# Optimization experiments

Hardware: AMD Instinct MI355X
Metric: run time of the kernel (lower is better)

## Reference

```python
import jax, jax.numpy as jnp
import numpy as np
import math

B, Q, CQ = 2, 2048, 512
H, D = 8, 64  # no_heads, c_hidden

def setup_inputs() -> dict:
    key = jax.random.key(0)
    ks = jax.random.split(key, 8)
    s = 0.02
    return {
        "q_x": jax.random.normal(ks[0], (B, Q, CQ), jnp.float32),
        "kv_x": jax.random.normal(ks[1], (B, Q, CQ), jnp.float32),
        "bias": jax.random.normal(ks[2], (B, 1, Q, Q), jnp.float32),
        "w_qkv": jax.random.normal(ks[3], (3 * H * D, CQ), jnp.float32) * s,
        "w_o": jax.random.normal(ks[4], (CQ, H * D), jnp.float32) * s,
        "b_o": jnp.zeros((CQ,), jnp.float32),
        "w_g": jax.random.normal(ks[5], (H * D, CQ), jnp.float32) * s,
        "b_g": jnp.zeros((H * D,), jnp.float32),
    }

def reference(q_x, kv_x, bias, w_qkv, w_o, b_o, w_g, b_g):
    # Fused QKV projection from q_x (kv_x is unused by the original module's _prep_qkv)
    qkv = jnp.einsum('bqc,ec->bqe', q_x, w_qkv)  # [B,Q,3*H*D]
    q, k, v = jnp.split(qkv, 3, axis=-1)
    q = q.reshape(B, Q, H, D) / math.sqrt(D)
    k = k.reshape(B, Q, H, D)
    v = v.reshape(B, Q, H, D)
    # scores + additive pairwise bias, softmax over keys
    scores = jnp.einsum('bqhd,bkhd->bhqk', q, k) + bias  # [B,H,Q,K]
    attn = jax.nn.softmax(scores, axis=-1)
    o = jnp.einsum('bhqk,bkhd->bqhd', attn, v)  # [B,Q,H,D]
    # sigmoid gating
    g = jax.nn.sigmoid(jnp.einsum('bqc,ec->bqe', q_x, w_g) + b_g).reshape(B, Q, H, D)
    o = o * g
    # output projection
    o = o.reshape(B, Q, H * D)
    return jnp.einsum('bqe,ce->bqc', o, w_o) + b_o
```

## Files before the change

### kernel.cpp

```cpp
#include <hip/hip_runtime.h>
#include <math.h>

#define B_  2
#define Q_  2048
#define CQ_ 512
#define H_  8
#define D_  64
#define M_  (B_*Q_)
#define L2E 1.44269504088896f

typedef __bf16 bf16;
typedef __bf16 bf16x4 __attribute__((ext_vector_type(4)));
typedef __bf16 bf16x8 __attribute__((ext_vector_type(8)));
typedef float  f32x4  __attribute__((ext_vector_type(4)));
typedef float  f32x16 __attribute__((ext_vector_type(16)));
typedef unsigned int u32x2 __attribute__((ext_vector_type(2)));

__device__ __forceinline__ void gl_lds16(const bf16* g, bf16* l) {
    __builtin_amdgcn_global_load_lds(
        (const __attribute__((address_space(1))) unsigned int*)g,
        (__attribute__((address_space(3))) unsigned int*)l, 16, 0, 0);
}

__device__ __forceinline__ unsigned int cvtpk_bf16(float lo, float hi) {
    unsigned int r;
    asm("v_cvt_pk_bf16_f32 %0, %1, %2" : "=v"(r) : "v"(lo), "v"(hi));
    return r;
}

#define S0 (4096*512)
#define S1 (1536*512)
#define S2 (512*512)
#define S3 (512*512)
#define NCV ((S0 + S1 + S2 + S3) / (256 * 8))
__global__ __launch_bounds__(256)
void convert_kernel(const float* __restrict__ qx, const float* __restrict__ wqkv,
                    const float* __restrict__ wg, const float* __restrict__ wo,
                    const float* __restrict__ bias,
                    bf16* __restrict__ qxb, bf16* __restrict__ wcat,
                    bf16* __restrict__ wob, float* __restrict__ bT)
{
    __shared__ float lds[2048];
    const int bx = blockIdx.x;
    const int t  = threadIdx.x;
    if (bx < NCV) {
        const long long e = ((long long)bx * 256 + t) * 8;
        const float* src; bf16* dst;
        if (e < S0)                { src = qx + e;                  dst = qxb + e; }
        else if (e < S0 + S1)      { src = wqkv + (e - S0);         dst = wcat + (e - S0); }
        else if (e < S0 + S1 + S2) { src = wg + (e - S0 - S1);      dst = wcat + S1 + (e - S0 - S1); }
        else                       { src = wo + (e - S0 - S1 - S2); dst = wob + (e - S0 - S1 - S2); }
        const float4 a = *(const float4*)(src);
        const float4 b = *(const float4*)(src + 4);
        bf16x8 v;
        v[0] = (bf16)a.x; v[1] = (bf16)a.y; v[2] = (bf16)a.z; v[3] = (bf16)a.w;
        v[4] = (bf16)b.x; v[5] = (bf16)b.y; v[6] = (bf16)b.z; v[7] = (bf16)b.w;
        *(bf16x8*)dst = v;
    } else {
        const int x = bx - NCV;
        const int b = x >> 11, q32 = (x >> 5) & 63, kt = x & 31;
        const int qo = t >> 3, kc = (t & 7) * 8;
        const float* src = bias + ((size_t)b * Q_ + q32 * 32 + qo) * Q_ + kt * 64 + kc;
        const float4 a = *(const float4*)src;
        const float4 c = *(const float4*)(src + 4);
        const float v[8] = {a.x, a.y, a.z, a.w, c.x, c.y, c.z, c.w};
        #pragma unroll
        for (int j2 = 0; j2 < 8; ++j2) {
            const int ko = kc + j2;
            const int i  = (ko >> 5) * 4 + ((ko >> 3) & 3);
            const int b5 = (ko >> 2) & 1;
            const int j  = ko & 3;
            lds[i * 256 + b5 * 128 + qo * 4 + j] = v[j2] * L2E;
        }
        __syncthreads();
        float* outp = bT + ((size_t)(b * 64 + q32) * 32 + kt) * 2048 + t * 8;
        *(float4*)(outp)     = *(const float4*)(lds + t * 8);
        *(float4*)(outp + 4) = *(const float4*)(lds + t * 8 + 4);
    }
}

template<int BM, int BN>
__global__ __launch_bounds__(256)
void gemm_bf16(const bf16* __restrict__ A, const bf16* __restrict__ W,
               const float* __restrict__ bvec,
               bf16* __restrict__ qb, bf16* __restrict__ kb, bf16* __restrict__ vb,
               bf16* __restrict__ gb)
{
    constexpr int MI = BM / 32, NJ = BN / 32;
    __shared__ __align__(16) bf16 As[BM * 32];
    __shared__ __align__(16) bf16 Bs[BN * 32];

    const int t = threadIdx.x;
    const int w = t >> 6, lane = t & 63;
    const int l15 = lane & 15, quad = lane >> 4;
    const int wm = w & 1, wn = w >> 1;
    const int bm = blockIdx.x * BM;
    const int bn = blockIdx.y * BN;
    const bool swapped = ((bn >> 9) != 2);

    f32x4 acc[MI][NJ] = {};

    const int rr = t >> 2;
    const int cc = (t & 3) * 8;

    for (int k0 = 0; k0 < 512; k0 += 32) {
        #pragma unroll
        for (int i = 0; i < BM / 64; ++i)
            gl_lds16(A + (size_t)(bm + i * 64 + rr) * 512 + k0 + cc,
                     As + (i * 64 + w * 16) * 32);
        #pragma unroll
        for (int i = 0; i < BN / 64; ++i)
            gl_lds16(W + (size_t)(bn + i * 64 + rr) * 512 + k0 + cc,
                     Bs + (i * 64 + w * 16) * 32);
        __asm__ volatile("s_waitcnt vmcnt(0)" ::: "memory");
        __syncthreads();

        bf16x8 af[MI], bfr[NJ];
        #pragma unroll
        for (int i = 0; i < MI; ++i)
            af[i] = *(const bf16x8*)(As + (wm * (BM / 2) + i * 16 + l15) * 32 + quad * 8);
        #pragma unroll
        for (int j = 0; j < NJ; ++j)
            bfr[j] = *(const bf16x8*)(Bs + (wn * (BN / 2) + j * 16 + l15) * 32 + quad * 8);
        if (swapped) {
            #pragma unroll
            for (int i = 0; i < MI; ++i)
                #pragma unroll
                for (int j = 0; j < NJ; ++j)
                    acc[i][j] = __builtin_amdgcn_mfma_f32_16x16x32_bf16(bfr[j], af[i], acc[i][j], 0, 0, 0);
        } else {
            #pragma unroll
            for (int i = 0; i < MI; ++i)
                #pragma unroll
                for (int j = 0; j < NJ; ++j)
                    acc[i][j] = __builtin_amdgcn_mfma_f32_16x16x32_bf16(af[i], bfr[j], acc[i][j], 0, 0, 0);
        }
        __syncthreads();
    }

    if (swapped) {
        #pragma unroll
        for (int i = 0; i < MI; ++i) {
            const int m = bm + wm * (BM / 2) + i * 16 + l15;
            const int b = m >> 11, qq = m & 2047;
            #pragma unroll
            for (int j = 0; j < NJ; ++j) {
                const int n0 = bn + wn * (BN / 2) + j * 16 + quad * 4;
                const f32x4 cv = acc[i][j];
                const int part = n0 >> 9;
                if (part == 0) {
                    const int h = (n0 >> 6) & 7, d0 = n0 & 63;
                    bf16x4 q4;
                    #pragma unroll
                    for (int r = 0; r < 4; ++r) q4[r] = (bf16)(cv[r] * (0.125f * L2E));
                    *(bf16x4*)(qb + (size_t)(b * H_ + h) * (Q_ * D_) + (size_t)qq * 64 + d0) = q4;
                } else if (part == 1) {
                    const int h = (n0 >> 6) & 7, d0 = n0 & 63;
                    const size_t off = (size_t)(b * H_ + h) * (Q_ * D_)
                        + (qq >> 6) * 4096 + ((qq >> 5) & 1) * 2048
                        + (d0 >> 4) * 512 + ((d0 >> 3) & 1) * 256
                        + (qq & 31) * 8 + (d0 & 7);
                    bf16x4 k4;
                    #pragma unroll
                    for (int r = 0; r < 4; ++r) k4[r] = (bf16)cv[r];
                    *(bf16x4*)(kb + off) = k4;
                } else {
                    const int gcol = n0 & 511;
                    const float4 bv4 = *(const float4*)(bvec + gcol);
                    bf16x4 g4;
                    g4[0] = (bf16)(1.f / (1.f + __expf(-(cv[0] + bv4.x))));
                    g4[1] = (bf16)(1.f / (1.f + __expf(-(cv[1] + bv4.y))));
                    g4[2] = (bf16)(1.f / (1.f + __expf(-(cv[2] + bv4.z))));
                    g4[3] = (bf16)(1.f / (1.f + __expf(-(cv[3] + bv4.w))));
                    *(bf16x4*)(gb + (size_t)m * 512 + gcol) = g4;
                }
            }
        }
    } else {
        #pragma unroll
        for (int i = 0; i < MI; ++i) {
            const int m0 = bm + wm * (BM / 2) + i * 16 + quad * 4;
            const int b = m0 >> 11, qq0 = m0 & 2047;
            #pragma unroll
            for (int j = 0; j < NJ; ++j) {
                const int n = bn + wn * (BN / 2) + j * 16 + l15;
                const int h = (n >> 6) & 7, d = n & 63;
                const size_t off = (size_t)(b * H_ + h) * (Q_ * D_)
                    + (qq0 >> 6) * 4096 + (d >> 5) * 2048
                    + ((qq0 & 63) >> 4) * 512 + ((qq0 >> 3) & 1) * 256
                    + (d & 31) * 8 + (qq0 & 7);
                bf16x4 v4;
                #pragma unroll
                for (int r = 0; r < 4; ++r) v4[r] = (bf16)acc[i][j][r];
                *(bf16x4*)(vb + off) = v4;
            }
        }
    }
}

__global__ __launch_bounds__(256, 3)
void attn_part(const bf16* __restrict__ qb, const bf16* __restrict__ kf,
               const bf16* __restrict__ vf, const float* __restrict__ bT,
               bf16* __restrict__ po, float2* __restrict__ ml)
{
    __shared__ __align__(16) bf16 Ks[2][4096];
    __shared__ __align__(16) bf16 Vs[2][4096];

    const int tid  = threadIdx.x;
    const int wv   = tid >> 6, lane = tid & 63;
    const int l31  = lane & 31, b5 = lane >> 5;
    const int x    = blockIdx.x;
    const int bh   = ((x & 7) << 1) | (x >> 3);
    const int b    = bh >> 3;
    const int qg   = blockIdx.y * 128 + wv * 32 + l31;
    const int ks   = blockIdx.z;
    const int t0   = ks * 11;
    const int nt   = (ks < 2) ? 11 : 10;

    const bf16* qp = qb + ((size_t)bh * Q_ + qg) * D_;
    bf16x8 bq[4];
    #pragma unroll
    for (int c = 0; c < 4; ++c)
        bq[c] = *(const bf16x8*)(qp + c * 16 + b5 * 8);

    f32x16 acc[2] = {};
    float m_run = -INFINITY, l_run = 0.f;

    const bf16*  kfb  = kf + (size_t)bh * (Q_ * D_) + (size_t)t0 * 4096;
    const bf16*  vfb  = vf + (size_t)bh * (Q_ * D_) + (size_t)t0 * 4096;
    const int q32 = blockIdx.y * 4 + wv;
    const float* brow = bT + (((size_t)b * 64 + q32) * 32 + t0) * 2048;

    f32x4 nb[8];

    #pragma unroll
    for (int p = 0; p < 2; ++p) {
        gl_lds16(kfb + (wv * 2 + p) * 512 + lane * 8, Ks[0] + (wv * 2 + p) * 512);
        gl_lds16(vfb + (wv * 2 + p) * 512 + lane * 8, Vs[0] + (wv * 2 + p) * 512);
    }
    #pragma unroll
    for (int i = 0; i < 8; ++i)
        nb[i] = *(const f32x4*)(brow + i * 256 + lane * 4);
    __asm__ volatile("s_waitcnt vmcnt(0)" ::: "memory");
    __syncthreads();

    int cur = 0;
    #pragma unroll 1
    for (int t = 0; t < nt; ++t) {
        if (t < nt - 1) {
            const size_t off = (size_t)(t + 1) * 4096;
            #pragma unroll
            for (int p = 0; p < 2; ++p) {
                gl_lds16(kfb + off + (wv * 2 + p) * 512 + lane * 8,
                         Ks[cur ^ 1] + (wv * 2 + p) * 512);
                gl_lds16(vfb + off + (wv * 2 + p) * 512 + lane * 8,
                         Vs[cur ^ 1] + (wv * 2 + p) * 512);
            }
        }
        __asm__ volatile("" ::: "memory");

        f32x16 sv[2];
        #pragma unroll
        for (int kg = 0; kg < 2; ++kg)
            #pragma unroll
            for (int r = 0; r < 16; ++r)
                sv[kg][r] = nb[kg * 4 + (r >> 2)][r & 3];

        if (t < nt - 1) {
            const float* bnx = brow + (size_t)(t + 1) * 2048;
            #pragma unroll
            for (int i = 0; i < 8; ++i)
                nb[i] = *(const f32x4*)(bnx + i * 256 + lane * 4);
        }
        __asm__ volatile("" ::: "memory");

        const bf16* Kc = Ks[cur];
        __builtin_amdgcn_s_setprio(1);
        #pragma unroll
        for (int kg = 0; kg < 2; ++kg)
            #pragma unroll
            for (int c = 0; c < 4; ++c) {
                const bf16x8 ak = *(const bf16x8*)(Kc + kg * 2048 + c * 512 + lane * 8);
                sv[kg] = __builtin_amdgcn_mfma_f32_32x32x16_bf16(ak, bq[c], sv[kg], 0, 0, 0);
            }
        __builtin_amdgcn_s_setprio(0);

        float mx[16];
        #pragma unroll
        for (int r = 0; r < 16; ++r) mx[r] = fmaxf(sv[0][r], sv[1][r]);
        #pragma unroll
        for (int r = 0; r < 8; ++r) mx[r] = fmaxf(mx[r], mx[r + 8]);
        #pragma unroll
        for (int r = 0; r < 4; ++r) mx[r] = fmaxf(mx[r], mx[r + 4]);
        float tmax = fmaxf(fmaxf(mx[0], mx[1]), fmaxf(mx[2], mx[3]));
        tmax = fmaxf(tmax, __shfl_xor(tmax, 32, 64));

        const float m_old = m_run;
        const bool keep = (__all(tmax <= m_old + 8.f) != 0);
        const float mn = keep ? m_old : fmaxf(m_old, tmax);
        m_run = mn;

        #pragma unroll
        for (int kg = 0; kg < 2; ++kg)
            #pragma unroll
            for (int r = 0; r < 16; ++r)
                sv[kg][r] = __builtin_amdgcn_exp2f(sv[kg][r] - mn);

        float sm[16];
        #pragma unroll
        for (int r = 0; r < 16; ++r) sm[r] = sv[0][r] + sv[1][r];
        #pragma unroll
        for (int r = 0; r < 8; ++r) sm[r] += sm[r + 8];
        #pragma unroll
        for (int r = 0; r < 4; ++r) sm[r] += sm[r + 4];
        float rsum = (sm[0] + sm[1]) + (sm[2] + sm[3]);
        rsum += __shfl_xor(rsum, 32, 64);
        if (keep) {
            l_run += rsum;
        } else {
            const float alpha = __builtin_amdgcn_exp2f(m_old - mn);
            l_run = l_run * alpha + rsum;
            acc[0] *= alpha;
            acc[1] *= alpha;
        }

        bf16x8 bp[4];
        #pragma unroll
        for (int kg = 0; kg < 2; ++kg)
            #pragma unroll
            for (int h = 0; h < 2; ++h) {
                const unsigned int u  = cvtpk_bf16(sv[kg][8 * h + 0], sv[kg][8 * h + 1]);
                const unsigned int u2 = cvtpk_bf16(sv[kg][8 * h + 2], sv[kg][8 * h + 3]);
                const unsigned int vv = cvtpk_bf16(sv[kg][8 * h + 4], sv[kg][8 * h + 5]);
                const unsigned int v2 = cvtpk_bf16(sv[kg][8 * h + 6], sv[kg][8 * h + 7]);
                const u32x2 s1 = __builtin_amdgcn_permlane32_swap(u,  vv, false, false);
                const u32x2 s2 = __builtin_amdgcn_permlane32_swap(u2, v2, false, false);
                union { unsigned int w[4]; bf16x8 v8; } pkw;
                pkw.w[0] = s1[0]; pkw.w[1] = s2[0]; pkw.w[2] = s1[1]; pkw.w[3] = s2[1];
                bp[kg * 2 + h] = pkw.v8;
            }

        const bf16* Vc = Vs[cur];
        __builtin_amdgcn_s_setprio(1);
        #pragma unroll
        for (int c4 = 0; c4 < 4; ++c4) {
            #pragma unroll
            for (int dg = 0; dg < 2; ++dg) {
                const bf16x8 av = *(const bf16x8*)(Vc + dg * 2048 + c4 * 512 + lane * 8);
                acc[dg] = __builtin_amdgcn_mfma_f32_32x32x16_bf16(av, bp[c4], acc[dg], 0, 0, 0);
            }
        }
        __builtin_amdgcn_s_setprio(0);

        __asm__ volatile("s_waitcnt vmcnt(8) lgkmcnt(0)" ::: "memory");
        __builtin_amdgcn_sched_barrier(0);
        __builtin_amdgcn_s_barrier();
        __builtin_amdgcn_sched_barrier(0);
        cur ^= 1;
    }

    const float inv = 1.f / l_run;
    const size_t pbase = ((size_t)(ks * 16 + bh) * Q_ + qg) * 64;
    #pragma unroll
    for (int dg = 0; dg < 2; ++dg)
        #pragma unroll
        for (int gi = 0; gi < 4; ++gi) {
            const int d0 = dg * 32 + gi * 8 + b5 * 4;
            bf16x4 ov;
            #pragma unroll
            for (int r = 0; r < 4; ++r)
                ov[r] = (bf16)(acc[dg][gi * 4 + r] * inv);
            *(bf16x4*)(po + pbase + d0) = ov;
        }
    if (b5 == 0)
        ml[(size_t)(ks * 16 + bh) * Q_ + qg] = make_float2(m_run, l_run);
}

__global__ __launch_bounds__(256)
void gemm_out(const bf16* __restrict__ po, const float2* __restrict__ ml,
              const bf16* __restrict__ gb, const bf16* __restrict__ W,
              const float* __restrict__ bvec, float* __restrict__ fout)
{
    constexpr int BM = 64, BN = 128, MI = BM / 32, NJ = BN / 32;
    __shared__ __align__(16) bf16 As[BM * 32];
    __shared__ __align__(16) bf16 Bs[BN * 32];

    const int t = threadIdx.x;
    const int w = t >> 6, lane = t & 63;
    const int l15 = lane & 15, quad = lane >> 4;
    const int wm = w & 1, wn = w >> 1;
    const int bm = blockIdx.x * BM;
    const int bn = blockIdx.y * BN;

    const int rr = t >> 2;
    const int cc = (t & 3) * 8;
    const int m  = bm + rr;
    const int b  = m >> 11, qq = m & 2047;

    f32x4 acc[MI][NJ] = {};

    float2 m0_, m1_, m2_;
    bf16x8 p0_, p1_, p2_, gv_;
    auto issueA = [&](int k0) {
        const int c0 = k0 + cc;
        const int h  = c0 >> 6, d8 = c0 & 63;
        const int prow = (b * 8 + h) * 2048 + qq;
        m0_ = ml[prow];
        m1_ = ml[32768 + prow];
        m2_ = ml[65536 + prow];
        p0_ = *(const bf16x8*)(po + (size_t)prow * 64 + d8);
        p1_ = *(const bf16x8*)(po + (size_t)(32768 + prow) * 64 + d8);
        p2_ = *(const bf16x8*)(po + (size_t)(65536 + prow) * 64 + d8);
        gv_ = *(const bf16x8*)(gb + (size_t)m * 512 + c0);
    };

    issueA(0);

    for (int k0 = 0; k0 < 512; k0 += 32) {
        #pragma unroll
        for (int i = 0; i < BN / 64; ++i)
            gl_lds16(W + (size_t)(bn + i * 64 + rr) * 512 + k0 + cc,
                     Bs + (i * 64 + w * 16) * 32);

        {
            const float Mx = fmaxf(fmaxf(m0_.x, m1_.x), m2_.x);
            float w0 = m0_.y * __builtin_amdgcn_exp2f(m0_.x - Mx);
            float w1 = m1_.y * __builtin_amdgcn_exp2f(m1_.x - Mx);
            float w2 = m2_.y * __builtin_amdgcn_exp2f(m2_.x - Mx);
            const float inv = 1.f / (w0 + w1 + w2);
            w0 *= inv; w1 *= inv; w2 *= inv;
            bf16x8 av;
            #pragma unroll
            for (int r = 0; r < 8; ++r)
                av[r] = (bf16)(((float)p0_[r] * w0 + (float)p1_[r] * w1 +
                                (float)p2_[r] * w2) * (float)gv_[r]);
            *(bf16x8*)(As + t * 8) = av;
        }
        __asm__ volatile("" ::: "memory");
        issueA(k0 + 32);
        __asm__ volatile("" ::: "memory");

        __asm__ volatile("s_waitcnt vmcnt(7) lgkmcnt(0)" ::: "memory");
        __builtin_amdgcn_sched_barrier(0);
        __builtin_amdgcn_s_barrier();
        __builtin_amdgcn_sched_barrier(0);

        bf16x8 af[MI], bfr[NJ];
        #pragma unroll
        for (int i = 0; i < MI; ++i)
            af[i] = *(const bf16x8*)(As + (wm * (BM / 2) + i * 16 + l15) * 32 + quad * 8);
        #pragma unroll
        for (int j = 0; j < NJ; ++j)
            bfr[j] = *(const bf16x8*)(Bs + (wn * (BN / 2) + j * 16 + l15) * 32 + quad * 8);
        #pragma unroll
        for (int i = 0; i < MI; ++i)
            #pragma unroll
            for (int j = 0; j < NJ; ++j)
                acc[i][j] = __builtin_amdgcn_mfma_f32_16x16x32_bf16(bfr[j], af[i], acc[i][j], 0, 0, 0);

        __asm__ volatile("s_waitcnt lgkmcnt(0)" ::: "memory");
        __builtin_amdgcn_sched_barrier(0);
        __builtin_amdgcn_s_barrier();
        __builtin_amdgcn_sched_barrier(0);
    }

    #pragma unroll
    for (int i = 0; i < MI; ++i) {
        const int mm = bm + wm * (BM / 2) + i * 16 + l15;
        #pragma unroll
        for (int j = 0; j < NJ; ++j) {
            const int n0 = bn + wn * (BN / 2) + j * 16 + quad * 4;
            const f32x4 cv = acc[i][j];
            float4 st;
            st.x = cv[0] + bvec[n0 + 0];
            st.y = cv[1] + bvec[n0 + 1];
            st.z = cv[2] + bvec[n0 + 2];
            st.w = cv[3] + bvec[n0 + 3];
            *(float4*)(fout + (size_t)mm * 512 + n0) = st;
        }
    }
}

extern "C" void kernel_launch(void* const* d_in, const int* in_sizes, int n_in,
                              void* d_out, int out_size, void* d_ws, size_t ws_size,
                              hipStream_t stream)
{
    const float* q_x   = (const float*)d_in[0];
    const float* bias  = (const float*)d_in[2];
    const float* w_qkv = (const float*)d_in[3];
    const float* w_o   = (const float*)d_in[4];
    const float* b_o   = (const float*)d_in[5];
    const float* w_g   = (const float*)d_in[6];
    const float* b_g   = (const float*)d_in[7];
    float* out = (float*)d_out;

    char* ws = (char*)d_ws;
    bf16*   qxb  = (bf16*)(ws);
    bf16*   wcat = (bf16*)(ws + (4u  << 20));
    bf16*   po   = (bf16*)(ws);
    bf16*   qb   = (bf16*)(ws + (16u << 20));
    bf16*   kb   = (bf16*)(ws + (20u << 20));
    bf16*   vb   = (bf16*)(ws + (24u << 20));
    bf16*   gb   = (bf16*)(ws + (28u << 20));
    bf16*   wob  = (bf16*)(ws + (36u << 20));
    float2* ml   = (float2*)(ws + (36u << 20) + (1u << 19));
    float*  bT   = (float*)(ws + (38u << 20));

    convert_kernel<<<NCV + B_ * 64 * 32, 256, 0, stream>>>(
        q_x, w_qkv, w_g, w_o, bias, qxb, wcat, wob, bT);
    gemm_bf16<128, 128><<<dim3(32, 16), 256, 0, stream>>>(
        qxb, wcat, b_g, qb, kb, vb, gb);
    attn_part<<<dim3(B_ * H_, Q_ / 128, 3), 256, 0, stream>>>(qb, kb, vb, bT, po, ml);
    gemm_out<<<dim3(64, 4), 256, 0, stream>>>(po, ml, gb, wob, b_o, out);
}
```

Measured before the change: 178.0 us.

## Split attention keys into four chunks with half-size tiles and higher occupancy

The attention kernel now splits the key dimension four ways instead of three, giving 1024 blocks instead of 768. Each iteration processes 32 keys instead of 64, which halves the LDS tiles and score registers and raises the launch-bounds occupancy target from 3 to 4. The output GEMM merges four partial results instead of three. In exchange there are more loop iterations with barriers, and more partial-output traffic to write and reduce.

```diff
diff --git a/kernel.cpp b/kernel.cpp
--- a/kernel.cpp
+++ b/kernel.cpp
@@ -198,13 +198,13 @@
     }
 }
 
-__global__ __launch_bounds__(256, 3)
+__global__ __launch_bounds__(256, 4)
 void attn_part(const bf16* __restrict__ qb, const bf16* __restrict__ kf,
                const bf16* __restrict__ vf, const float* __restrict__ bT,
                bf16* __restrict__ po, float2* __restrict__ ml)
 {
-    __shared__ __align__(16) bf16 Ks[2][4096];
-    __shared__ __align__(16) bf16 Vs[2][4096];
+    __shared__ __align__(16) bf16 Ks[2][2048];
+    __shared__ __align__(16) bf16 Vs[2][2048];
 
     const int tid  = threadIdx.x;
     const int wv   = tid >> 6, lane = tid & 63;
@@ -214,8 +214,7 @@
     const int b    = bh >> 3;
     const int qg   = blockIdx.y * 128 + wv * 32 + l31;
     const int ks   = blockIdx.z;
-    const int t0   = ks * 11;
-    const int nt   = (ks < 2) ? 11 : 10;
+    const int nt   = 16;
 
     const bf16* qp = qb + ((size_t)bh * Q_ + qg) * D_;
     bf16x8 bq[4];
@@ -226,20 +225,19 @@
     f32x16 acc[2] = {};
     float m_run = -INFINITY, l_run = 0.f;
 
-    const bf16*  kfb  = kf + (size_t)bh * (Q_ * D_) + (size_t)t0 * 4096;
-    const bf16*  vfb  = vf + (size_t)bh * (Q_ * D_) + (size_t)t0 * 4096;
+    const bf16*  kfb  = kf + (size_t)bh * (Q_ * D_) + (size_t)ks * 8 * 4096;
+    const bf16*  vfb  = vf + (size_t)bh * (Q_ * D_) + (size_t)ks * 8 * 4096;
     const int q32 = blockIdx.y * 4 + wv;
-    const float* brow = bT + (((size_t)b * 64 + q32) * 32 + t0) * 2048;
-
-    f32x4 nb[8];
-
+    const float* brow = bT + (((size_t)b * 64 + q32) * 32 + ks * 8) * 2048;
+
+    const int vwo = ((wv & 2) ? 2048 : 0) + (wv & 1) * 512;
+
+    f32x4 nb[4];
+
+    gl_lds16(kfb + wv * 512 + lane * 8, Ks[0] + wv * 512);
+    gl_lds16(vfb + vwo + lane * 8, Vs[0] + wv * 512);
     #pragma unroll
-    for (int p = 0; p < 2; ++p) {
-        gl_lds16(kfb + (wv * 2 + p) * 512 + lane * 8, Ks[0] + (wv * 2 + p) * 512);
-        gl_lds16(vfb + (wv * 2 + p) * 512 + lane * 8, Vs[0] + (wv * 2 + p) * 512);
-    }
-    #pragma unroll
-    for (int i = 0; i < 8; ++i)
+    for (int i = 0; i < 4; ++i)
         nb[i] = *(const f32x4*)(brow + i * 256 + lane * 4);
     __asm__ volatile("s_waitcnt vmcnt(0)" ::: "memory");
     __syncthreads();
@@ -248,28 +246,24 @@
     #pragma unroll 1
     for (int t = 0; t < nt; ++t) {
         if (t < nt - 1) {
-            const size_t off = (size_t)(t + 1) * 4096;
-            #pragma unroll
-            for (int p = 0; p < 2; ++p) {
-                gl_lds16(kfb + off + (wv * 2 + p) * 512 + lane * 8,
-                         Ks[cur ^ 1] + (wv * 2 + p) * 512);
-                gl_lds16(vfb + off + (wv * 2 + p) * 512 + lane * 8,
-                         Vs[cur ^ 1] + (wv * 2 + p) * 512);
-            }
+            const int tn = t + 1;
+            const size_t kb_t = (size_t)(tn >> 1) * 4096 + (tn & 1) * 2048;
+            const size_t vb_t = (size_t)(tn >> 1) * 4096 + (tn & 1) * 1024;
+            gl_lds16(kfb + kb_t + wv * 512 + lane * 8, Ks[cur ^ 1] + wv * 512);
+            gl_lds16(vfb + vb_t + vwo + lane * 8, Vs[cur ^ 1] + wv * 512);
         }
         __asm__ volatile("" ::: "memory");
 
-        f32x16 sv[2];
-        #pragma unroll
-        for (int kg = 0; kg < 2; ++kg)
-            #pragma unroll
-            for (int r = 0; r < 16; ++r)
-                sv[kg][r] = nb[kg * 4 + (r >> 2)][r & 3];
+        f32x16 sv;
+        #pragma unroll
+        for (int r = 0; r < 16; ++r)
+            sv[r] = nb[r >> 2][r & 3];
 
         if (t < nt - 1) {
-            const float* bnx = brow + (size_t)(t + 1) * 2048;
-            #pragma unroll
-            for (int i = 0; i < 8; ++i)
+            const int tn = t + 1;
+            const float* bnx = brow + (size_t)(tn >> 1) * 2048 + (tn & 1) * 1024;
+            #pragma unroll
+            for (int i = 0; i < 4; ++i)
                 nb[i] = *(const f32x4*)(bnx + i * 256 + lane * 4);
         }
         __asm__ volatile("" ::: "memory");
@@ -277,19 +271,15 @@
         const bf16* Kc = Ks[cur];
         __builtin_amdgcn_s_setprio(1);
         #pragma unroll
-        for (int kg = 0; kg < 2; ++kg)
-            #pragma unroll
-            for (int c = 0; c < 4; ++c) {
-                const bf16x8 ak = *(const bf16x8*)(Kc + kg * 2048 + c * 512 + lane * 8);
-                sv[kg] = __builtin_amdgcn_mfma_f32_32x32x16_bf16(ak, bq[c], sv[kg], 0, 0, 0);
-            }
+        for (int c = 0; c < 4; ++c) {
+            const bf16x8 ak = *(const bf16x8*)(Kc + c * 512 + lane * 8);
+            sv = __builtin_amdgcn_mfma_f32_32x32x16_bf16(ak, bq[c], sv, 0, 0, 0);
+        }
         __builtin_amdgcn_s_setprio(0);
 
-        float mx[16];
-        #pragma unroll
-        for (int r = 0; r < 16; ++r) mx[r] = fmaxf(sv[0][r], sv[1][r]);
-        #pragma unroll
-        for (int r = 0; r < 8; ++r) mx[r] = fmaxf(mx[r], mx[r + 8]);
+        float mx[8];
+        #pragma unroll
+        for (int r = 0; r < 8; ++r) mx[r] = fmaxf(sv[r], sv[r + 8]);
         #pragma unroll
         for (int r = 0; r < 4; ++r) mx[r] = fmaxf(mx[r], mx[r + 4]);
         float tmax = fmaxf(fmaxf(mx[0], mx[1]), fmaxf(mx[2], mx[3]));
@@ -301,16 +291,12 @@
         m_run = mn;
 
         #pragma unroll
-        for (int kg = 0; kg < 2; ++kg)
-            #pragma unroll
-            for (int r = 0; r < 16; ++r)
-                sv[kg][r] = __builtin_amdgcn_exp2f(sv[kg][r] - mn);
-
-        float sm[16];
-        #pragma unroll
-        for (int r = 0; r < 16; ++r) sm[r] = sv[0][r] + sv[1][r];
-        #pragma unroll
-        for (int r = 0; r < 8; ++r) sm[r] += sm[r + 8];
+        for (int r = 0; r < 16; ++r)
+            sv[r] = __builtin_amdgcn_exp2f(sv[r] - mn);
+
+        float sm[8];
+        #pragma unroll
+        for (int r = 0; r < 8; ++r) sm[r] = sv[r] + sv[r + 8];
         #pragma unroll
         for (int r = 0; r < 4; ++r) sm[r] += sm[r + 4];
         float rsum = (sm[0] + sm[1]) + (sm[2] + sm[3]);
@@ -324,35 +310,33 @@
             acc[1] *= alpha;
         }
 
-        bf16x8 bp[4];
-        #pragma unroll
-        for (int kg = 0; kg < 2; ++kg)
-            #pragma unroll
-            for (int h = 0; h < 2; ++h) {
-                const unsigned int u  = cvtpk_bf16(sv[kg][8 * h + 0], sv[kg][8 * h + 1]);
-                const unsigned int u2 = cvtpk_bf16(sv[kg][8 * h + 2], sv[kg][8 * h + 3]);
-                const unsigned int vv = cvtpk_bf16(sv[kg][8 * h + 4], sv[kg][8 * h + 5]);
-                const unsigned int v2 = cvtpk_bf16(sv[kg][8 * h + 6], sv[kg][8 * h + 7]);
-                const u32x2 s1 = __builtin_amdgcn_permlane32_swap(u,  vv, false, false);
-                const u32x2 s2 = __builtin_amdgcn_permlane32_swap(u2, v2, false, false);
-                union { unsigned int w[4]; bf16x8 v8; } pkw;
-                pkw.w[0] = s1[0]; pkw.w[1] = s2[0]; pkw.w[2] = s1[1]; pkw.w[3] = s2[1];
-                bp[kg * 2 + h] = pkw.v8;
-            }
+        bf16x8 bp[2];
+        #pragma unroll
+        for (int h = 0; h < 2; ++h) {
+            const unsigned int u  = cvtpk_bf16(sv[8 * h + 0], sv[8 * h + 1]);
+            const unsigned int u2 = cvtpk_bf16(sv[8 * h + 2], sv[8 * h + 3]);
+            const unsigned int vv = cvtpk_bf16(sv[8 * h + 4], sv[8 * h + 5]);
+            const unsigned int v2 = cvtpk_bf16(sv[8 * h + 6], sv[8 * h + 7]);
+            const u32x2 s1 = __builtin_amdgcn_permlane32_swap(u,  vv, false, false);
+            const u32x2 s2 = __builtin_amdgcn_permlane32_swap(u2, v2, false, false);
+            union { unsigned int w[4]; bf16x8 v8; } pkw;
+            pkw.w[0] = s1[0]; pkw.w[1] = s2[0]; pkw.w[2] = s1[1]; pkw.w[3] = s2[1];
+            bp[h] = pkw.v8;
+        }
 
         const bf16* Vc = Vs[cur];
         __builtin_amdgcn_s_setprio(1);
         #pragma unroll
-        for (int c4 = 0; c4 < 4; ++c4) {
+        for (int kc = 0; kc < 2; ++kc) {
             #pragma unroll
             for (int dg = 0; dg < 2; ++dg) {
-                const bf16x8 av = *(const bf16x8*)(Vc + dg * 2048 + c4 * 512 + lane * 8);
-                acc[dg] = __builtin_amdgcn_mfma_f32_32x32x16_bf16(av, bp[c4], acc[dg], 0, 0, 0);
+                const bf16x8 av = *(const bf16x8*)(Vc + dg * 1024 + kc * 512 + lane * 8);
+                acc[dg] = __builtin_amdgcn_mfma_f32_32x32x16_bf16(av, bp[kc], acc[dg], 0, 0, 0);
             }
         }
         __builtin_amdgcn_s_setprio(0);
 
-        __asm__ volatile("s_waitcnt vmcnt(8) lgkmcnt(0)" ::: "memory");
+        __asm__ volatile("s_waitcnt vmcnt(4) lgkmcnt(0)" ::: "memory");
         __builtin_amdgcn_sched_barrier(0);
         __builtin_amdgcn_s_barrier();
         __builtin_amdgcn_sched_barrier(0);
@@ -399,8 +383,8 @@
 
     f32x4 acc[MI][NJ] = {};
 
-    float2 m0_, m1_, m2_;
-    bf16x8 p0_, p1_, p2_, gv_;
+    float2 m0_, m1_, m2_, m3_;
+    bf16x8 p0_, p1_, p2_, p3_, gv_;
     auto issueA = [&](int k0) {
         const int c0 = k0 + cc;
         const int h  = c0 >> 6, d8 = c0 & 63;
@@ -408,9 +392,11 @@
         m0_ = ml[prow];
         m1_ = ml[32768 + prow];
         m2_ = ml[65536 + prow];
+        m3_ = ml[98304 + prow];
         p0_ = *(const bf16x8*)(po + (size_t)prow * 64 + d8);
         p1_ = *(const bf16x8*)(po + (size_t)(32768 + prow) * 64 + d8);
         p2_ = *(const bf16x8*)(po + (size_t)(65536 + prow) * 64 + d8);
+        p3_ = *(const bf16x8*)(po + (size_t)(98304 + prow) * 64 + d8);
         gv_ = *(const bf16x8*)(gb + (size_t)m * 512 + c0);
     };
 
@@ -423,24 +409,25 @@
                      Bs + (i * 64 + w * 16) * 32);
 
         {
-            const float Mx = fmaxf(fmaxf(m0_.x, m1_.x), m2_.x);
+            const float Mx = fmaxf(fmaxf(m0_.x, m1_.x), fmaxf(m2_.x, m3_.x));
             float w0 = m0_.y * __builtin_amdgcn_exp2f(m0_.x - Mx);
             float w1 = m1_.y * __builtin_amdgcn_exp2f(m1_.x - Mx);
             float w2 = m2_.y * __builtin_amdgcn_exp2f(m2_.x - Mx);
-            const float inv = 1.f / (w0 + w1 + w2);
-            w0 *= inv; w1 *= inv; w2 *= inv;
+            float w3 = m3_.y * __builtin_amdgcn_exp2f(m3_.x - Mx);
+            const float inv = 1.f / (w0 + w1 + w2 + w3);
+            w0 *= inv; w1 *= inv; w2 *= inv; w3 *= inv;
             bf16x8 av;
             #pragma unroll
             for (int r = 0; r < 8; ++r)
                 av[r] = (bf16)(((float)p0_[r] * w0 + (float)p1_[r] * w1 +
-                                (float)p2_[r] * w2) * (float)gv_[r]);
+                                (float)p2_[r] * w2 + (float)p3_[r] * w3) * (float)gv_[r]);
             *(bf16x8*)(As + t * 8) = av;
         }
         __asm__ volatile("" ::: "memory");
         issueA(k0 + 32);
         __asm__ volatile("" ::: "memory");
 
-        __asm__ volatile("s_waitcnt vmcnt(7) lgkmcnt(0)" ::: "memory");
+        __asm__ volatile("s_waitcnt vmcnt(9) lgkmcnt(0)" ::: "memory");
         __builtin_amdgcn_sched_barrier(0);
         __builtin_amdgcn_s_barrier();
         __builtin_amdgcn_sched_barrier(0);
@@ -510,6 +497,6 @@
         q_x, w_qkv, w_g, w_o, bias, qxb, wcat, wob, bT);
     gemm_bf16<128, 128><<<dim3(32, 16), 256, 0, stream>>>(
         qxb, wcat, b_g, qb, kb, vb, gb);
-    attn_part<<<dim3(B_ * H_, Q_ / 128, 3), 256, 0, stream>>>(qb, kb, vb, bT, po, ml);
+    attn_part<<<dim3(B_ * H_, Q_ / 128, 4), 256, 0, stream>>>(qb, kb, vb, bT, po, ml);
     gemm_out<<<dim3(64, 4), 256, 0, stream>>>(po, ml, gb, wob, b_o, out);
 }
```

New measurement: 184.8 us. 3.8% more time.
